# Kernel optimization log

Measured on AMD Instinct MI355X. Metric: run time of the kernel, lower is better.

## Reference

```python
import jax, jax.numpy as jnp
from jax import lax
import numpy as np

BN_EPS = 1e-5

def _bn(x, g, b, m, v):
    # inference-mode BatchNorm1d (running stats)
    return (x - m) * (g / jnp.sqrt(v + BN_EPS)) + b

def _mlp2(x, W1, g, b, m, v, W2):
    # Linear(no bias) -> BN -> ReLU -> (Dropout off in eval) -> Linear(no bias)
    h = jax.nn.relu(_bn(x @ W1.T, g, b, m, v))
    return h @ W2.T

def setup_inputs() -> dict:
    key = jax.random.key(0)
    ks = iter(jax.random.split(key, 40))
    B, N = 1024, 10
    f32 = jnp.float32
    def w(shape, s=0.02):
        return jax.random.normal(next(ks), shape, f32) * s
    def bn_params(c):
        return (jnp.ones((c,), f32), jnp.zeros((c,), f32),
                jax.random.normal(next(ks), (c,), f32) * 0.1,
                jax.random.uniform(next(ks), (c,), f32, 0.5, 1.5))
    inp = {
        'features_object': jax.random.normal(next(ks), (B, N, 1024), f32),
        'bbox': jax.random.uniform(next(ks), (B, N, 4), f32),
        'word_embedding': jax.random.normal(next(ks), (B, N, 300), f32),
        'sentiment': jax.random.normal(next(ks), (B, N, 4096), f32),
        'body': jax.random.normal(next(ks), (B, 2048), f32),
    }
    # mlp_object: 1024 -> 128 -> 128
    inp['W1_o'] = w((128, 1024)); inp['g_o'], inp['b_o'], inp['m_o'], inp['v_o'] = bn_params(128)
    inp['W2_o'] = w((128, 128))
    # mlp_sentiment: 4096 -> 512 -> 128
    inp['W1_s'] = w((512, 4096)); inp['g_s'], inp['b_s'], inp['m_s'], inp['v_s'] = bn_params(512)
    inp['W2_s'] = w((128, 512))
    # mlp_body: 2048 -> 256 -> 128
    inp['W1_b'] = w((256, 2048)); inp['g_b'], inp['b_b'], inp['m_b'], inp['v_b'] = bn_params(256)
    inp['W2_b'] = w((128, 256))
    # channel attention (CBAM-style, in_planes=10, ratio=2): shared MLP 10->5->10
    inp['Wc1'] = w((5, 10), 0.3)
    inp['Wc2'] = w((10, 5), 0.3)
    # spatial attention: Conv1d(2 -> 1, k=7, pad=3, no bias)
    inp['Wsa'] = w((1, 2, 7), 0.3)
    # fc1: 688 -> 256 (with bias) then BN
    inp['Wf'] = w((256, 688)); inp['bf'] = jnp.zeros((256,), f32)
    inp['g_f'], inp['b_f'], inp['m_f'], inp['v_f'] = bn_params(256)
    return inp

def reference(features_object, bbox, word_embedding, sentiment, body,
              W1_o, g_o, b_o, m_o, v_o, W2_o,
              W1_s, g_s, b_s, m_s, v_s, W2_s,
              W1_b, g_b, b_b, m_b, v_b, W2_b,
              Wc1, Wc2, Wsa, Wf, bf, g_f, b_f, m_f, v_f):
    B, N, _ = features_object.shape
    # per-slice MLPs batched into single GEMMs over B*N rows
    obj = _mlp2(features_object.reshape(B * N, -1), W1_o, g_o, b_o, m_o, v_o, W2_o).reshape(B, N, 128)
    sen = _mlp2(sentiment.reshape(B * N, -1), W1_s, g_s, b_s, m_s, v_s, W2_s).reshape(B, N, 128)
    # body is identical across the N repeats (inference BN), compute once and broadcast
    bod = _mlp2(body.reshape(B, -1), W1_b, g_b, b_b, m_b, v_b, W2_b)
    bod = jnp.broadcast_to(bod[:, None, :], (B, N, 128))
    x = jnp.concatenate([obj, bbox, word_embedding, sen, bod], axis=2)  # [B,N,688]
    # channel attention over the N-slice axis
    def ca_mlp(a):  # [B,N] -> [B,N]
        return jax.nn.relu(a @ Wc1.T) @ Wc2.T
    att_c = jax.nn.sigmoid(ca_mlp(x.mean(axis=2)) + ca_mlp(x.max(axis=2)))  # [B,N]
    x = x * att_c[:, :, None]
    # spatial attention along feature axis
    s = jnp.stack([x.mean(axis=1), x.max(axis=1)], axis=1)  # [B,2,688]
    sa = lax.conv_general_dilated(s, Wsa, (1,), [(3, 3)],
                                  dimension_numbers=('NCH', 'OIH', 'NCH'))  # [B,1,688]
    x = x * jax.nn.sigmoid(sa)
    x = x.sum(axis=1)  # [B,688]
    out = jax.nn.relu(_bn(x @ Wf.T + bf, g_f, b_f, m_f, v_f))  # [B,256]
    return out
```

## Files before the change

### kernel.cpp

```cpp
#include <hip/hip_runtime.h>
#include <hip/hip_bf16.h>
#include <math.h>

typedef __attribute__((ext_vector_type(8))) short short8;
typedef __attribute__((ext_vector_type(4))) float floatx4;

static __device__ __forceinline__ unsigned short f2bf(float f) {
    unsigned int u = __float_as_uint(f);
    unsigned int r = (u + 0x7fffu + ((u >> 16) & 1u)) >> 16;
    return (unsigned short)r;
}

static __device__ __forceinline__ unsigned int pk_bf16(float lo, float hi) {
    unsigned int r;
    asm("v_cvt_pk_bf16_f32 %0, %1, %2" : "=v"(r) : "v"(lo), "v"(hi));
    return r;
}

static __device__ __forceinline__ void g2l16(const void* g, void* l) {
    __builtin_amdgcn_global_load_lds(
        (const __attribute__((address_space(1))) unsigned int*)g,
        (__attribute__((address_space(3))) unsigned int*)l,
        16, 0, 0);
}

struct GDesc {
    const float*          Af;
    const unsigned short* Ab;
    const unsigned short* W;
    float*          Cf;
    unsigned short* Cb;
    const float *bias, *g, *b, *m, *v;
    int M, N, K;
    int Kreal;
    int fuse;
    int nbx;
    int block0;
    int nbb;
    int ksplit;
};
struct GArgs { GDesc g[3]; int n; };

__global__ __launch_bounds__(256)
void gemm_grouped(GArgs ga)
{
    __shared__ unsigned short As[2][4096];
    __shared__ unsigned short Bs[2][4096];

    const int bid = blockIdx.x;
    int gi = 0;
    #pragma unroll
    for (int i = 1; i < 3; ++i)
        if (i < ga.n && bid >= ga.g[i].block0) gi = i;
    const GDesc d = ga.g[gi];

    int local = bid - d.block0;
    int kc = 0;
    int Kc = d.K;
    if (d.ksplit > 1) {
        Kc = d.K / d.ksplit;
        kc = local / d.nbb;
        local -= kc * d.nbb;
    }
    const int kbeg = kc * Kc;
    const int bx = local % d.nbx;
    const int by = local / d.nbx;
    const int row0 = by * 128;
    const int col0 = bx * 128;

    const int tid  = threadIdx.x;
    const int wave = tid >> 6;
    const int lane = tid & 63;
    const int qd   = lane >> 4;
    const int ln   = lane & 15;
    const int wr   = (wave >> 1) * 64;
    const int wc   = (wave & 1) * 64;

    const int c0 = wave * 128 + lane;
    const int c1 = c0 + 64;
    const int r0 = c0 >> 2, k0 = (c0 & 3) * 8;
    const int r1 = c1 >> 2, k1 = (c1 & 3) * 8;

    const int sr = tid >> 3;
    const int sc = (tid & 7) * 4;

    const bool afp = (d.Af != nullptr);
    const int niter = Kc >> 5;

    floatx4 acc[4][4];
    #pragma unroll
    for (int i = 0; i < 4; ++i)
        #pragma unroll
        for (int j = 0; j < 4; ++j) acc[i][j] = (floatx4){0.f, 0.f, 0.f, 0.f};

    g2l16(d.W + (size_t)(col0 + r0) * d.K + kbeg + k0, &Bs[0][(size_t)wave * 1024]);
    g2l16(d.W + (size_t)(col0 + r1) * d.K + kbeg + k1, &Bs[0][(size_t)wave * 1024 + 512]);
    float4 areg[4];
    if (afp) {
        #pragma unroll
        for (int p = 0; p < 4; ++p) {
            float4 v = (kbeg + sc < d.Kreal)
                ? *(const float4*)(d.Af + (size_t)(row0 + p * 32 + sr) * d.Kreal + kbeg + sc)
                : (float4){0.f, 0.f, 0.f, 0.f};
            uint2 o = { pk_bf16(v.x, v.y), pk_bf16(v.z, v.w) };
            *(uint2*)&As[0][(p * 32 + sr) * 32 + sc] = o;
        }
        if (niter > 1) {
            const int kg = kbeg + 32;
            #pragma unroll
            for (int p = 0; p < 4; ++p)
                areg[p] = (kg + sc < d.Kreal)
                    ? *(const float4*)(d.Af + (size_t)(row0 + p * 32 + sr) * d.Kreal + kg + sc)
                    : (float4){0.f, 0.f, 0.f, 0.f};
        }
    } else {
        g2l16(d.Ab + (size_t)(row0 + r0) * d.K + kbeg + k0, &As[0][(size_t)wave * 1024]);
        g2l16(d.Ab + (size_t)(row0 + r1) * d.K + kbeg + k1, &As[0][(size_t)wave * 1024 + 512]);
    }
    __syncthreads();

    int cur = 0;
    for (int it = 0; it < niter; ++it) {
        const int nxt = cur ^ 1;
        const bool pf = (it + 1 < niter);

        if (pf) {
            const int kg = kbeg + (it + 1) * 32;
            g2l16(d.W + (size_t)(col0 + r0) * d.K + kg + k0, &Bs[nxt][(size_t)wave * 1024]);
            g2l16(d.W + (size_t)(col0 + r1) * d.K + kg + k1, &Bs[nxt][(size_t)wave * 1024 + 512]);
            if (afp) {
                #pragma unroll
                for (int p = 0; p < 4; ++p) {
                    uint2 o = { pk_bf16(areg[p].x, areg[p].y),
                                pk_bf16(areg[p].z, areg[p].w) };
                    *(uint2*)&As[nxt][(p * 32 + sr) * 32 + sc] = o;
                }
                if (it + 2 < niter) {
                    const int kg2 = kbeg + (it + 2) * 32;
                    #pragma unroll
                    for (int p = 0; p < 4; ++p)
                        areg[p] = (kg2 + sc < d.Kreal)
                            ? *(const float4*)(d.Af + (size_t)(row0 + p * 32 + sr) * d.Kreal + kg2 + sc)
                            : (float4){0.f, 0.f, 0.f, 0.f};
                }
            } else {
                g2l16(d.Ab + (size_t)(row0 + r0) * d.K + kg + k0, &As[nxt][(size_t)wave * 1024]);
                g2l16(d.Ab + (size_t)(row0 + r1) * d.K + kg + k1, &As[nxt][(size_t)wave * 1024 + 512]);
            }
        }

        short8 a[4], b[4];
        #pragma unroll
        for (int i = 0; i < 4; ++i)
            a[i] = *(const short8*)&As[cur][(wr + i * 16 + ln) * 32 + qd * 8];
        #pragma unroll
        for (int j = 0; j < 4; ++j)
            b[j] = *(const short8*)&Bs[cur][(wc + j * 16 + ln) * 32 + qd * 8];
        #pragma unroll
        for (int i = 0; i < 4; ++i)
            #pragma unroll
            for (int j = 0; j < 4; ++j)
                acc[i][j] = __builtin_amdgcn_mfma_f32_16x16x32_bf16(
                                a[i], b[j], acc[i][j], 0, 0, 0);

        __syncthreads();
        cur = nxt;
    }

    if (d.ksplit > 1) {
        #pragma unroll
        for (int j = 0; j < 4; ++j) {
            const int col = col0 + wc + j * 16 + ln;
            #pragma unroll
            for (int i = 0; i < 4; ++i) {
                #pragma unroll
                for (int r = 0; r < 4; ++r) {
                    const int row = row0 + wr + i * 16 + qd * 4 + r;
                    atomicAdd(&d.Cf[(size_t)row * d.N + col], acc[i][j][r]);
                }
            }
        }
        return;
    }

    #pragma unroll
    for (int j = 0; j < 4; ++j) {
        const int col = col0 + wc + j * 16 + ln;
        float add = d.bias ? d.bias[col] : 0.f;
        float scale = 1.f, shift = 0.f;
        if (d.fuse) {
            scale = d.g[col] * rsqrtf(d.v[col] + 1e-5f);
            shift = d.b[col] - d.m[col] * scale;
        }
        #pragma unroll
        for (int i = 0; i < 4; ++i) {
            #pragma unroll
            for (int r = 0; r < 4; ++r) {
                const int row = row0 + wr + i * 16 + qd * 4 + r;
                float vv = acc[i][j][r] + add;
                if (d.fuse) vv = fmaxf(vv * scale + shift, 0.f);
                if (d.Cf) d.Cf[(size_t)row * d.N + col] = vv;
                if (d.Cb) d.Cb[(size_t)row * d.N + col] = f2bf(vv);
            }
        }
    }
}

struct WSeg { const float* src; unsigned short* dst; int Kreal; int Kp; };
struct WArgs { WSeg s[7]; int off[8]; float4* zdst; int zn; };

__global__ __launch_bounds__(256)
void cvt_weights(WArgs wa)
{
    int i = blockIdx.x * 256 + threadIdx.x;
    if (i >= wa.off[7]) {
        int z = i - wa.off[7];
        if (z < wa.zn) wa.zdst[z] = (float4){0.f, 0.f, 0.f, 0.f};
        return;
    }
    int s = 0;
    #pragma unroll
    for (int j = 1; j < 7; ++j) if (i >= wa.off[j]) s = j;
    const WSeg sg = wa.s[s];
    const int li = i - wa.off[s];
    const int r = li / sg.Kp, c = li - r * sg.Kp;
    sg.dst[li] = (c < sg.Kreal) ? f2bf(sg.src[(size_t)r * sg.Kreal + c])
                                : (unsigned short)0;
}

struct FSeg { const float* src; unsigned short* dstb; float* dstf;
              const float *bias, *g, *b, *m, *v; int N; };
struct FArgs { FSeg s[3]; int off[4]; };

__global__ __launch_bounds__(256)
void bn_finalize(FArgs fa)
{
    int i = blockIdx.x * 256 + threadIdx.x;
    if (i >= fa.off[3]) return;
    int s = 0;
    #pragma unroll
    for (int j = 1; j < 3; ++j) if (i >= fa.off[j]) s = j;
    const FSeg sg = fa.s[s];
    const int li = i - fa.off[s];
    const int e = li * 4;
    const int col = e % sg.N;
    float4 vv = *(const float4*)(sg.src + e);
    float4 fo;
    ushort4 o;
    #pragma unroll
    for (int r = 0; r < 4; ++r) {
        float x = (&vv.x)[r];
        if (sg.bias) x += sg.bias[col + r];
        float sc = sg.g[col + r] * rsqrtf(sg.v[col + r] + 1e-5f);
        float sh = sg.b[col + r] - sg.m[col + r] * sc;
        x = fmaxf(x * sc + sh, 0.f);
        (&fo.x)[r] = x;
        ((unsigned short*)&o)[r] = f2bf(x);
    }
    if (sg.dstb) *(ushort4*)(sg.dstb + e) = o;
    if (sg.dstf) *(float4*)(sg.dstf + e) = fo;
}

__global__ __launch_bounds__(256)
void attn_kernel(const float* __restrict__ obj, const float* __restrict__ bbox,
                 const float* __restrict__ word, const float* __restrict__ sen,
                 const float* __restrict__ bod,
                 const float* __restrict__ Wc1, const float* __restrict__ Wc2,
                 const float* __restrict__ Wsa,
                 float* __restrict__ xsum_out)
{
    const int b = blockIdx.x;
    const int tid = threadIdx.x;

    __shared__ float xs[10][688];
    __shared__ float s0[688], s1[688];
    __shared__ float avec[10], mvec[10], att[10];
    __shared__ float cw[14], c1[50], c2[50];

    if (tid < 14) cw[tid] = Wsa[tid];
    if (tid < 50) { c1[tid] = Wc1[tid]; c2[tid] = Wc2[tid]; }

    for (int n = 0; n < 10; ++n) {
        const float* o  = obj  + ((size_t)b * 10 + n) * 128;
        const float* bx = bbox + ((size_t)b * 10 + n) * 4;
        const float* w  = word + ((size_t)b * 10 + n) * 300;
        const float* s  = sen  + ((size_t)b * 10 + n) * 128;
        const float* bo = bod  + (size_t)b * 128;
        for (int c = tid; c < 688; c += 256) {
            float v;
            if      (c < 128) v = o[c];
            else if (c < 132) v = bx[c - 128];
            else if (c < 432) v = w[c - 132];
            else if (c < 560) v = s[c - 432];
            else              v = bo[c - 560];
            xs[n][c] = v;
        }
    }
    __syncthreads();

    {
        const int wv = tid >> 6, ln2 = tid & 63;
        for (int n = wv; n < 10; n += 4) {
            float sm = 0.f, mx = -INFINITY;
            for (int c = ln2; c < 688; c += 64) {
                float v = xs[n][c];
                sm += v; mx = fmaxf(mx, v);
            }
            #pragma unroll
            for (int off = 32; off > 0; off >>= 1) {
                sm += __shfl_down(sm, off);
                mx = fmaxf(mx, __shfl_down(mx, off));
            }
            if (ln2 == 0) { avec[n] = sm * (1.f / 688.f); mvec[n] = mx; }
        }
    }
    __syncthreads();

    if (tid == 0) {
        float ha[5], hm[5];
        #pragma unroll
        for (int i = 0; i < 5; ++i) {
            float sa_ = 0.f, sm_ = 0.f;
            #pragma unroll
            for (int j = 0; j < 10; ++j) {
                sa_ += c1[i * 10 + j] * avec[j];
                sm_ += c1[i * 10 + j] * mvec[j];
            }
            ha[i] = fmaxf(sa_, 0.f);
            hm[i] = fmaxf(sm_, 0.f);
        }
        #pragma unroll
        for (int j = 0; j < 10; ++j) {
            float v = 0.f;
            #pragma unroll
            for (int i = 0; i < 5; ++i) v += c2[j * 5 + i] * (ha[i] + hm[i]);
            att[j] = 1.f / (1.f + expf(-v));
        }
    }
    __syncthreads();

    for (int c = tid; c < 688; c += 256) {
        float sm = 0.f, mx = -INFINITY;
        #pragma unroll
        for (int n = 0; n < 10; ++n) {
            float v = xs[n][c] * att[n];
            xs[n][c] = v;
            sm += v; mx = fmaxf(mx, v);
        }
        s0[c] = sm * 0.1f;
        s1[c] = mx;
    }
    __syncthreads();

    for (int c = tid; c < 688; c += 256) {
        float sa = 0.f;
        #pragma unroll
        for (int j = 0; j < 7; ++j) {
            int cc = c + j - 3;
            if (cc >= 0 && cc < 688)
                sa += cw[j] * s0[cc] + cw[7 + j] * s1[cc];
        }
        float sig = 1.f / (1.f + expf(-sa));
        float sm = 0.f;
        #pragma unroll
        for (int n = 0; n < 10; ++n) sm += xs[n][c];
        xsum_out[(size_t)b * 688 + c] = sm * sig;
    }
}

extern "C" void kernel_launch(void* const* d_in, const int* in_sizes, int n_in,
                              void* d_out, int out_size, void* d_ws, size_t ws_size,
                              hipStream_t stream)
{
    const float* f_obj = (const float*)d_in[0];
    const float* bbox  = (const float*)d_in[1];
    const float* word  = (const float*)d_in[2];
    const float* sent  = (const float*)d_in[3];
    const float* body  = (const float*)d_in[4];
    const float* W1_o  = (const float*)d_in[5];
    const float* g_o = (const float*)d_in[6],  *b_o = (const float*)d_in[7];
    const float* m_o = (const float*)d_in[8],  *v_o = (const float*)d_in[9];
    const float* W2_o  = (const float*)d_in[10];
    const float* W1_s  = (const float*)d_in[11];
    const float* g_s = (const float*)d_in[12], *b_s = (const float*)d_in[13];
    const float* m_s = (const float*)d_in[14], *v_s = (const float*)d_in[15];
    const float* W2_s  = (const float*)d_in[16];
    const float* W1_b  = (const float*)d_in[17];
    const float* g_b = (const float*)d_in[18], *b_b = (const float*)d_in[19];
    const float* m_b = (const float*)d_in[20], *v_b = (const float*)d_in[21];
    const float* W2_b  = (const float*)d_in[22];
    const float* Wc1 = (const float*)d_in[23];
    const float* Wc2 = (const float*)d_in[24];
    const float* Wsa = (const float*)d_in[25];
    const float* Wf  = (const float*)d_in[26];
    const float* bf  = (const float*)d_in[27];
    const float* g_f = (const float*)d_in[28], *b_f = (const float*)d_in[29];
    const float* m_f = (const float*)d_in[30], *v_f = (const float*)d_in[31];
    float* out = (float*)d_out;

    char* p = (char*)d_ws;
    unsigned short* w1s = (unsigned short*)p; p += 4194304;
    unsigned short* w2s = (unsigned short*)p; p += 131072;
    unsigned short* w1o = (unsigned short*)p; p += 262144;
    unsigned short* w2o = (unsigned short*)p; p += 32768;
    unsigned short* w1b = (unsigned short*)p; p += 1048576;
    unsigned short* w2b = (unsigned short*)p; p += 65536;
    unsigned short* wfp = (unsigned short*)p; p += 360448;
    unsigned short* h_s = (unsigned short*)p; p += 10485760;
    unsigned short* h_o = (unsigned short*)p; p += 2621440;
    unsigned short* h_b = (unsigned short*)p; p += 524288;
    char* region = p; p += 27262976;
    float* ps = (float*)region;
    float* po = (float*)(region + 20971520);
    float* pb = (float*)(region + 26214400);
    float* sen_f  = (float*)region;
    float* obj_f  = (float*)(region + 5242880);
    float* bod_f  = (float*)(region + 10485760);
    float* xsum_f = (float*)(region + 11010048);
    if ((size_t)(p - (char*)d_ws) > ws_size) return;

    WArgs wa;
    wa.s[0] = { W1_s, w1s, 4096, 4096 };
    wa.s[1] = { W2_s, w2s,  512,  512 };
    wa.s[2] = { W1_o, w1o, 1024, 1024 };
    wa.s[3] = { W2_o, w2o,  128,  128 };
    wa.s[4] = { W1_b, w1b, 2048, 2048 };
    wa.s[5] = { W2_b, w2b,  256,  256 };
    wa.s[6] = { Wf,   wfp,  688,  704 };
    const int wn[7] = { 512*4096, 128*512, 128*1024, 128*128, 256*2048, 128*256, 256*704 };
    wa.off[0] = 0;
    for (int i = 0; i < 7; ++i) wa.off[i + 1] = wa.off[i] + wn[i];
    wa.zdst = (float4*)region;
    wa.zn   = 27262976 / 16;
    cvt_weights<<<(wa.off[7] + wa.zn + 255) / 256, 256, 0, stream>>>(wa);

    {
        GArgs ga; ga.n = 3;
        ga.g[0] = { sent,  nullptr, w1s, ps, nullptr, nullptr, nullptr, nullptr, nullptr, nullptr,
                    10240, 512, 4096, 4096, 0, 4, 0,   320, 2 };
        ga.g[1] = { f_obj, nullptr, w1o, po, nullptr, nullptr, nullptr, nullptr, nullptr, nullptr,
                    10240, 128, 1024, 1024, 0, 1, 640, 80,  2 };
        ga.g[2] = { body,  nullptr, w1b, pb, nullptr, nullptr, nullptr, nullptr, nullptr, nullptr,
                    1024,  256, 2048, 2048, 0, 2, 800, 16,  2 };
        gemm_grouped<<<832, 256, 0, stream>>>(ga);
    }

    {
        FArgs fa;
        fa.s[0] = { ps, h_s, nullptr, nullptr, g_s, b_s, m_s, v_s, 512 };
        fa.s[1] = { po, h_o, nullptr, nullptr, g_o, b_o, m_o, v_o, 128 };
        fa.s[2] = { pb, h_b, nullptr, nullptr, g_b, b_b, m_b, v_b, 256 };
        fa.off[0] = 0;
        fa.off[1] = 10240 * 512 / 4;
        fa.off[2] = fa.off[1] + 10240 * 128 / 4;
        fa.off[3] = fa.off[2] + 1024 * 256 / 4;
        bn_finalize<<<(fa.off[3] + 255) / 256, 256, 0, stream>>>(fa);
    }

    {
        GArgs ga; ga.n = 3;
        ga.g[0] = { nullptr, h_s, w2s, sen_f, nullptr, nullptr, nullptr, nullptr, nullptr, nullptr,
                    10240, 128, 512, 512, 0, 1, 0,   80, 1 };
        ga.g[1] = { nullptr, h_o, w2o, obj_f, nullptr, nullptr, nullptr, nullptr, nullptr, nullptr,
                    10240, 128, 128, 128, 0, 1, 80,  80, 1 };
        ga.g[2] = { nullptr, h_b, w2b, bod_f, nullptr, nullptr, nullptr, nullptr, nullptr, nullptr,
                    1024,  128, 256, 256, 0, 1, 160, 8,  1 };
        gemm_grouped<<<168, 256, 0, stream>>>(ga);
    }

    attn_kernel<<<1024, 256, 0, stream>>>(obj_f, bbox, word, sen_f, bod_f,
                                          Wc1, Wc2, Wsa, xsum_f);

    {
        GArgs ga; ga.n = 1;
        ga.g[0] = { xsum_f, nullptr, wfp, out, nullptr, bf, g_f, b_f, m_f, v_f,
                    1024, 256, 704, 688, 1, 2, 0, 16, 1 };
        gemm_grouped<<<16, 256, 0, stream>>>(ga);
    }
}
```

Before: 537.6 us.

## Stream fp32 A tiles directly to LDS and convert at fragment load; remap blocks

```diff
diff --git a/kernel.cpp b/kernel.cpp
--- a/kernel.cpp
+++ b/kernel.cpp
@@ -44,8 +44,9 @@
 __global__ __launch_bounds__(256)
 void gemm_grouped(GArgs ga)
 {
-    __shared__ unsigned short As[2][4096];
+    __shared__ float          As_f[2][4096];
     __shared__ unsigned short Bs[2][4096];
+    unsigned short* As_b = (unsigned short*)&As_f[0][0];
 
     const int bid = blockIdx.x;
     int gi = 0;
@@ -55,6 +56,10 @@
     const GDesc d = ga.g[gi];
 
     int local = bid - d.block0;
+    {
+        const int cpx = (d.nbb * d.ksplit) >> 3;
+        local = (local & 7) * cpx + (local >> 3);
+    }
     int kc = 0;
     int Kc = d.K;
     if (d.ksplit > 1) {
@@ -81,8 +86,8 @@
     const int r0 = c0 >> 2, k0 = (c0 & 3) * 8;
     const int r1 = c1 >> 2, k1 = (c1 & 3) * 8;
 
-    const int sr = tid >> 3;
-    const int sc = (tid & 7) * 4;
+    const int aro  = wave * 32 + (lane >> 3);
+    const int acol = (lane & 7) * 4;
 
     const bool afp = (d.Af != nullptr);
     const int niter = Kc >> 5;
@@ -95,27 +100,14 @@
 
     g2l16(d.W + (size_t)(col0 + r0) * d.K + kbeg + k0, &Bs[0][(size_t)wave * 1024]);
     g2l16(d.W + (size_t)(col0 + r1) * d.K + kbeg + k1, &Bs[0][(size_t)wave * 1024 + 512]);
-    float4 areg[4];
     if (afp) {
         #pragma unroll
-        for (int p = 0; p < 4; ++p) {
-            float4 v = (kbeg + sc < d.Kreal)
-                ? *(const float4*)(d.Af + (size_t)(row0 + p * 32 + sr) * d.Kreal + kbeg + sc)
-                : (float4){0.f, 0.f, 0.f, 0.f};
-            uint2 o = { pk_bf16(v.x, v.y), pk_bf16(v.z, v.w) };
-            *(uint2*)&As[0][(p * 32 + sr) * 32 + sc] = o;
-        }
-        if (niter > 1) {
-            const int kg = kbeg + 32;
-            #pragma unroll
-            for (int p = 0; p < 4; ++p)
-                areg[p] = (kg + sc < d.Kreal)
-                    ? *(const float4*)(d.Af + (size_t)(row0 + p * 32 + sr) * d.Kreal + kg + sc)
-                    : (float4){0.f, 0.f, 0.f, 0.f};
-        }
+        for (int t = 0; t < 4; ++t)
+            g2l16(d.Af + (size_t)(row0 + aro + t * 8) * d.Kreal + kbeg + acol,
+                  &As_f[0][(size_t)(wave * 4 + t) * 256]);
     } else {
-        g2l16(d.Ab + (size_t)(row0 + r0) * d.K + kbeg + k0, &As[0][(size_t)wave * 1024]);
-        g2l16(d.Ab + (size_t)(row0 + r1) * d.K + kbeg + k1, &As[0][(size_t)wave * 1024 + 512]);
+        g2l16(d.Ab + (size_t)(row0 + r0) * d.K + kbeg + k0, As_b + (size_t)wave * 1024);
+        g2l16(d.Ab + (size_t)(row0 + r1) * d.K + kbeg + k1, As_b + (size_t)wave * 1024 + 512);
     }
     __syncthreads();
 
@@ -130,29 +122,31 @@
             g2l16(d.W + (size_t)(col0 + r1) * d.K + kg + k1, &Bs[nxt][(size_t)wave * 1024 + 512]);
             if (afp) {
                 #pragma unroll
-                for (int p = 0; p < 4; ++p) {
-                    uint2 o = { pk_bf16(areg[p].x, areg[p].y),
-                                pk_bf16(areg[p].z, areg[p].w) };
-                    *(uint2*)&As[nxt][(p * 32 + sr) * 32 + sc] = o;
-                }
-                if (it + 2 < niter) {
-                    const int kg2 = kbeg + (it + 2) * 32;
-                    #pragma unroll
-                    for (int p = 0; p < 4; ++p)
-                        areg[p] = (kg2 + sc < d.Kreal)
-                            ? *(const float4*)(d.Af + (size_t)(row0 + p * 32 + sr) * d.Kreal + kg2 + sc)
-                            : (float4){0.f, 0.f, 0.f, 0.f};
-                }
+                for (int t = 0; t < 4; ++t)
+                    g2l16(d.Af + (size_t)(row0 + aro + t * 8) * d.Kreal + kg + acol,
+                          &As_f[nxt][(size_t)(wave * 4 + t) * 256]);
             } else {
-                g2l16(d.Ab + (size_t)(row0 + r0) * d.K + kg + k0, &As[nxt][(size_t)wave * 1024]);
-                g2l16(d.Ab + (size_t)(row0 + r1) * d.K + kg + k1, &As[nxt][(size_t)wave * 1024 + 512]);
+                g2l16(d.Ab + (size_t)(row0 + r0) * d.K + kg + k0, As_b + (size_t)nxt * 4096 + wave * 1024);
+                g2l16(d.Ab + (size_t)(row0 + r1) * d.K + kg + k1, As_b + (size_t)nxt * 4096 + wave * 1024 + 512);
             }
         }
 
         short8 a[4], b[4];
-        #pragma unroll
-        for (int i = 0; i < 4; ++i)
-            a[i] = *(const short8*)&As[cur][(wr + i * 16 + ln) * 32 + qd * 8];
+        if (afp) {
+            #pragma unroll
+            for (int i = 0; i < 4; ++i) {
+                const float* ap = &As_f[cur][(wr + i * 16 + ln) * 32 + qd * 8];
+                float4 v0 = *(const float4*)ap;
+                float4 v1 = *(const float4*)(ap + 4);
+                int4 pk = { (int)pk_bf16(v0.x, v0.y), (int)pk_bf16(v0.z, v0.w),
+                            (int)pk_bf16(v1.x, v1.y), (int)pk_bf16(v1.z, v1.w) };
+                a[i] = *(short8*)&pk;
+            }
+        } else {
+            #pragma unroll
+            for (int i = 0; i < 4; ++i)
+                a[i] = *(const short8*)&As_b[(size_t)cur * 4096 + (wr + i * 16 + ln) * 32 + qd * 8];
+        }
         #pragma unroll
         for (int j = 0; j < 4; ++j)
             b[j] = *(const short8*)&Bs[cur][(wc + j * 16 + ln) * 32 + qd * 8];
```

Result: faster. 522.4 us (-2.8%).
